# Performance work log

Hardware: AMD Instinct MI355X
Metric: run time of the kernel (lower is better)

## Reference

```python
import jax, jax.numpy as jnp
import numpy as np

H = 32; W = 32; C = 128; K = 3
FS = K * K                      # filter_size = 9
CH = H - K + 1; CW = W - K + 1
F = CH * CW                     # num_convs = 900
HW = H * W                      # 1024
TEMP = 1.0                      # softmax_temp
EPS = 1e-5                      # masked_softmax epsilon
B = 8


def _build_masks():
    # local_indices[f] = flat indices of the K x K window f (row-major),
    # matching compute_input_mask with stride=1, no stochastic stride.
    idx = np.zeros((F, FS), dtype=np.int32)
    f = 0
    for i in range(CH):
        for j in range(CW):
            rows = np.arange(i, i + K)[:, None]
            cols = np.arange(j, j + K)[None, :]
            idx[f] = (rows * W + cols).reshape(-1)
            f += 1
    # global mask = (1 - local_mask) * (1 - padding_mask); padding_mask == 0 for 'valid'
    gmask = np.ones((F, HW), dtype=np.float32)
    gmask[np.arange(F)[:, None], idx] = 0.0
    return jnp.asarray(idx), jnp.asarray(gmask)


def setup_inputs() -> dict:
    key = jax.random.key(0)
    ks = jax.random.split(key, 8)
    bound = 1.0 / np.sqrt(C)  # torch nn.Linear default init
    u = lambda k, shape: jax.random.uniform(k, shape, jnp.float32, -bound, bound)
    batch = jax.random.normal(ks[0], (B, H, W, C), jnp.float32)
    Wq = u(ks[1], (C, C)); bq = u(ks[2], (C,))
    Wk = u(ks[3], (C, C)); bk = u(ks[4], (C,))
    wv = u(ks[5], (C, 1)); bv = u(ks[6], (1,))
    local_indices, gmask = _build_masks()
    return {"batch": batch, "Wq": Wq, "bq": bq, "Wk": Wk, "bk": bk,
            "wv": wv, "bv": bv, "gmask": gmask, "local_indices": local_indices}


def reference(batch, Wq, bq, Wk, bk, wv, bv, gmask, local_indices):
    # Approach '4': per-window local queries attend over global (non-window)
    # pixels; scalar values gate the local patch pixels; gated patch sums to
    # one output pixel per window. Valid padding => local pixels are unmasked
    # and the masked softmax zeroes out window/padding positions, so the
    # per-window masked linear transforms reduce exactly to full-image
    # transforms gathered/masked afterwards (no [F,B,H,W,C] materialization).
    b = batch.shape[0]
    xf = batch.reshape(b, HW, C)
    Q = xf @ Wq.T + bq                         # [B,HW,C] query_transform
    Kf = xf @ Wk.T + bk                        # [B,HW,C] key_transform
    V = (xf @ wv + bv)[..., 0]                 # [B,HW]   value_transform (C->1)
    Qg = Q[:, local_indices]                   # [B,F,FS,C] local queries (gather)
    Xl = xf[:, local_indices]                  # [B,F,FS,C] local patch features
    compat = jnp.einsum('bfpc,bqc->bfpq', Qg, Kf) / TEMP   # [B,F,FS,HW]
    # masked_softmax: exp * mask / (sum + eps), no max-subtraction (faithful)
    exps = jnp.exp(compat) * gmask[None, :, None, :]
    attn = exps / (exps.sum(-1, keepdims=True) + EPS)
    gates = jnp.einsum('bfpq,bq->bfp', attn, V)            # [B,F,FS] scalar gates
    out = jnp.einsum('bfp,bfpc->bfc', gates, Xl)           # [B,F,C]
    return out.reshape(b, CH, CW, C)
```

## Files before the change

### kernel.cpp

```cpp
#include <hip/hip_runtime.h>

#define BATCH 8
#define HW_N  1024
#define CD    128
#define W_IMG 32
#define CH_O  30
#define F_N   900

#define OFF_Q16 0u
#define OFF_K16 2097152u
#define OFF_V   4194304u
#define OFF_D   4227072u
#define OFF_TP  5046272u
#define OFF_TVP 5570560u
#define OFF_WQF 6094848u
#define OFF_WKF 6127616u

typedef _Float16 f16x8 __attribute__((ext_vector_type(8)));
typedef _Float16 f16x4 __attribute__((ext_vector_type(4)));
typedef float    f32x4 __attribute__((ext_vector_type(4)));

__device__ __forceinline__ size_t frag_off(int R, int k) {
    return (size_t)(R >> 4) * 2048 +
           (size_t)((((k >> 5) * 4 + ((k >> 3) & 3)) * 128) + ((R & 15) * 8) + (k & 7));
}

__device__ __forceinline__ void async16(const void* g, void* l) {
    __builtin_amdgcn_global_load_lds(
        (const __attribute__((address_space(1))) unsigned int*)g,
        (__attribute__((address_space(3))) unsigned int*)l,
        16, 0, 0);
}

__global__ __launch_bounds__(256) void prep_kernel(
    const float* __restrict__ Wq, const float* __restrict__ Wk,
    _Float16* __restrict__ WqF, _Float16* __restrict__ WkF)
{
    int id = blockIdx.x * 256 + threadIdx.x;
    int c  = id >> 4;
    int kc = id & 15;
    size_t src = (size_t)c * CD + kc * 8;
    size_t dst = frag_off(c, kc * 8);

    float vq[8], vk[8];
    *(float4*)&vq[0] = *(const float4*)&Wq[src];
    *(float4*)&vq[4] = *(const float4*)&Wq[src + 4];
    *(float4*)&vk[0] = *(const float4*)&Wk[src];
    *(float4*)&vk[4] = *(const float4*)&Wk[src + 4];

    f16x8 qh, kh;
#pragma unroll
    for (int e = 0; e < 8; ++e) {
        qh[e] = (_Float16)vq[e];
        kh[e] = (_Float16)vk[e];
    }
    *(f16x8*)&WqF[dst] = qh;
    *(f16x8*)&WkF[dst] = kh;
}

__global__ __launch_bounds__(256) void qkv_kernel(
    const float* __restrict__ xf,
    const float* __restrict__ bq, const float* __restrict__ bk,
    const float* __restrict__ wv, const float* __restrict__ bv,
    const _Float16* __restrict__ WqF, const _Float16* __restrict__ WkF,
    _Float16* __restrict__ Q16, _Float16* __restrict__ K16,
    float* __restrict__ V)
{
    __shared__ float    xs[16][132];
    __shared__ _Float16 xh[2048];

    const int t = threadIdx.x;
    const int rowbase = blockIdx.x * 16;

#pragma unroll
    for (int m = 0; m < 2; ++m) {
        int id = t + 256 * m;
        int r  = id >> 5;
        int c4 = id & 31;
        float4 v4 = *(const float4*)&xf[(size_t)(rowbase + r) * CD + c4 * 4];
        *(float4*)&xs[r][c4 * 4] = v4;
        int c = c4 * 4;
        int off = ((c >> 5) * 4 + ((c >> 3) & 3)) * 128 + r * 8 + (c & 7);
        f16x4 hh;
        hh[0] = (_Float16)v4.x; hh[1] = (_Float16)v4.y;
        hh[2] = (_Float16)v4.z; hh[3] = (_Float16)v4.w;
        *(f16x4*)&xh[off] = hh;
    }
    __syncthreads();

    const int w    = t >> 6;
    const int lane = t & 63;
    const int q    = lane >> 4;
    const int i    = lane & 15;

    f32x4 aq[2], ak[2];
#pragma unroll
    for (int ct = 0; ct < 2; ++ct) {
        aq[ct] = (f32x4){0.f, 0.f, 0.f, 0.f};
        ak[ct] = (f32x4){0.f, 0.f, 0.f, 0.f};
    }

#pragma unroll
    for (int ks = 0; ks < 4; ++ks) {
        const int aoff = (ks * 4 + q) * 128 + i * 8;
        f16x8 ah = *(f16x8*)&xh[aoff];
#pragma unroll
        for (int ct = 0; ct < 2; ++ct) {
            size_t boff = (size_t)(w * 2 + ct) * 2048 + (size_t)(ks * 4 + q) * 128 + i * 8;
            f16x8 bq8 = *(const f16x8*)&WqF[boff];
            f16x8 bk8 = *(const f16x8*)&WkF[boff];
            aq[ct] = __builtin_amdgcn_mfma_f32_16x16x32_f16(ah, bq8, aq[ct], 0, 0, 0);
            ak[ct] = __builtin_amdgcn_mfma_f32_16x16x32_f16(ah, bk8, ak[ct], 0, 0, 0);
        }
    }

#pragma unroll
    for (int ct = 0; ct < 2; ++ct) {
        int c = (w * 2 + ct) * 16 + i;
        float bqv = bq[c], bkv = bk[c];
#pragma unroll
        for (int g = 0; g < 4; ++g) {
            int R = rowbase + q * 4 + g;
            size_t o = frag_off(R, c);
            Q16[o] = (_Float16)(aq[ct][g] + bqv);
            K16[o] = (_Float16)(ak[ct][g] + bkv);
        }
    }

    if (t < 16) {
        float s = 0.f;
#pragma unroll 8
        for (int k = 0; k < CD; ++k) s += xs[t][k] * wv[k];
        V[rowbase + t] = s + bv[0];
    }
}

#define A_OFF 0
#define B_OFF 16384
#define VS_OFF 32768
#define SCR2 16896
#define ATTN_LDS_TOTAL 33792

__global__ __launch_bounds__(256) void attn_kernel(
    const _Float16* __restrict__ Q16, const _Float16* __restrict__ K16,
    const float* __restrict__ V,
    double* __restrict__ Tp, double* __restrict__ TVp,
    float* __restrict__ D)
{
    extern __shared__ char lds[];
    _Float16* Ah = (_Float16*)(lds + A_OFF);
    _Float16* Bh = (_Float16*)(lds + B_OFF);
    float*    Vs = (float*)(lds + VS_OFF);

    const int b  = blockIdx.x;
    const int rb = blockIdx.y;
    const int cb = blockIdx.z;
    const int t  = threadIdx.x;
    const int w    = t >> 6;
    const int lane = t & 63;
    const int q    = lane >> 4;
    const int i    = lane & 15;
    const int wy = w >> 1, wx = w & 1;

    if (t < 128) Vs[t] = V[b * HW_N + cb * 128 + t];

    f32x4 acc[4][4];
#pragma unroll
    for (int r = 0; r < 4; ++r)
#pragma unroll
        for (int f = 0; f < 4; ++f) acc[r][f] = (f32x4){0.f, 0.f, 0.f, 0.f};

    const size_t abase = (size_t)(b * 8 + rb) * 16384;
    const size_t bbase = (size_t)(b * 8 + cb) * 16384;

    for (int kh = 0; kh < 2; ++kh) {
        __syncthreads();
#pragma unroll
        for (int m = 0; m < 4; ++m) {
            int id = t + 256 * m;
            size_t goff = (size_t)(id >> 7) * 2048 + kh * 1024 + (id & 127) * 8;
            int loff = id * 8;
            async16(Q16 + abase + goff, Ah + loff);
            async16(K16 + bbase + goff, Bh + loff);
        }
        asm volatile("s_waitcnt vmcnt(0)" ::: "memory");
        __syncthreads();

#pragma unroll
        for (int kcl = 0; kcl < 2; ++kcl) {
            f16x8 a4[4], b4[4];
#pragma unroll
            for (int r = 0; r < 4; ++r) {
                int ao = (((wy * 4 + r) * 2 + kcl) * 4 + q) * 128 + i * 8;
                a4[r] = *(f16x8*)&Ah[ao];
                int bo = (((wx * 4 + r) * 2 + kcl) * 4 + q) * 128 + i * 8;
                b4[r] = *(f16x8*)&Bh[bo];
            }
#pragma unroll
            for (int r = 0; r < 4; ++r)
#pragma unroll
                for (int f = 0; f < 4; ++f)
                    acc[r][f] = __builtin_amdgcn_mfma_f32_16x16x32_f16(
                        a4[r], b4[f], acc[r][f], 0, 0, 0);
        }
    }

    float st[4][4], stv[4][4];
#pragma unroll
    for (int r = 0; r < 4; ++r)
#pragma unroll
        for (int g = 0; g < 4; ++g) { st[r][g] = 0.f; stv[r][g] = 0.f; }

    const bool band = (cb - rb <= 1) && (rb - cb <= 1);

#pragma unroll
    for (int f = 0; f < 4; ++f) {
        int col_local = wx * 64 + f * 16 + i;
        int hw_c = cb * 128 + col_local;
        float v = Vs[col_local];
        int cimg_r = hw_c >> 5, cimg_c = hw_c & 31;
#pragma unroll
        for (int r = 0; r < 4; ++r)
#pragma unroll
            for (int g = 0; g < 4; ++g) {
                float e = __expf(acc[r][f][g]);
                st[r][g]  += e;
                stv[r][g] += e * v;
                if (band) {
                    int row_local = wy * 64 + r * 16 + q * 4 + g;
                    int hw_r = rb * 128 + row_local;
                    int dy = cimg_r - (hw_r >> 5);
                    int dx = cimg_c - (hw_r & 31);
                    if ((unsigned)(dy + 2) <= 4u && (unsigned)(dx + 2) <= 4u)
                        D[(size_t)(b * HW_N + hw_r) * 25 + (dy + 2) * 5 + (dx + 2)] = e;
                }
            }
    }

    __syncthreads();
    float* scrT  = (float*)lds;
    float* scrTV = (float*)(lds + SCR2);
#pragma unroll
    for (int r = 0; r < 4; ++r)
#pragma unroll
        for (int g = 0; g < 4; ++g) {
            int rl = wy * 64 + r * 16 + q * 4 + g;
            scrT [rl * 33 + wx * 16 + i] = st[r][g];
            scrTV[rl * 33 + wx * 16 + i] = stv[r][g];
        }
    __syncthreads();
    if (t < 128) {
        double s = 0.0;
#pragma unroll
        for (int c = 0; c < 32; ++c) s += (double)scrT[t * 33 + c];
        Tp[(size_t)(b * HW_N + rb * 128 + t) * 8 + cb] = s;
    } else {
        int tt = t - 128;
        double s = 0.0;
#pragma unroll
        for (int c = 0; c < 32; ++c) s += (double)scrTV[tt * 33 + c];
        TVp[(size_t)(b * HW_N + rb * 128 + tt) * 8 + cb] = s;
    }
}

__global__ __launch_bounds__(256) void gate_out_kernel(
    const float* __restrict__ xf, const float* __restrict__ V,
    const double* __restrict__ Tp, const double* __restrict__ TVp,
    const float* __restrict__ D, float* __restrict__ out)
{
    const int fi = blockIdx.x;
    const int b  = blockIdx.y;
    const int t  = threadIdx.x;

    __shared__ float  xs[96 * 128];
    __shared__ float  gates[32][9];
    __shared__ double Ts[96], TVs[96];

#pragma unroll
    for (int m = 0; m < 12; ++m) {
        int id   = t + 256 * m;
        int srow = id >> 5;
        int c4   = id & 31;
        int r3   = srow >> 5, colc = srow & 31;
        *(float4*)&xs[srow * 128 + c4 * 4] =
            *(const float4*)&xf[((size_t)(b * 32 + fi + r3) * 32 + colc) * CD + c4 * 4];
    }

    if (t < 96) {
        int R = b * HW_N + (fi + (t >> 5)) * W_IMG + (t & 31);
        double s = 0.0;
#pragma unroll
        for (int c = 0; c < 8; ++c) s += Tp[(size_t)R * 8 + c];
        Ts[t] = s;
    } else if (t >= 128 && t < 224) {
        int tt = t - 128;
        int R = b * HW_N + (fi + (tt >> 5)) * W_IMG + (tt & 31);
        double s = 0.0;
#pragma unroll
        for (int c = 0; c < 8; ++c) s += TVp[(size_t)R * 8 + c];
        TVs[tt] = s;
    }
    __syncthreads();

    for (int g = t; g < 270; g += 256) {
        int fj = g / 9, p = g % 9;
        int pr = p / 3, pc = p % 3;
        int lrow = pr * 32 + fj + pc;
        int ip = (fi + pr) * W_IMG + (fj + pc);
        const float* Drow = &D[(size_t)(b * HW_N + ip) * 25];
        double se = 0.0, sev = 0.0;
#pragma unroll
        for (int qq = 0; qq < 9; ++qq) {
            int qr = qq / 3, qc = qq % 3;
            float e = Drow[(qr - pr + 2) * 5 + (qc - pc + 2)];
            se  += (double)e;
            sev += (double)(e * V[b * HW_N + (fi + qr) * W_IMG + (fj + qc)]);
        }
        double denom = Ts[lrow] - se + 1e-5;
        double numer = TVs[lrow] - sev;
        gates[fj][p] = (float)(numer / denom);
    }
    __syncthreads();

    const int c4  = t & 31;
    const int fjl = t >> 5;
#pragma unroll
    for (int it = 0; it < 4; ++it) {
        int fj = fjl + 8 * it;
        if (fj < CH_O) {
            f32x4 o = (f32x4){0.f, 0.f, 0.f, 0.f};
#pragma unroll
            for (int p = 0; p < 9; ++p) {
                int pr = p / 3, pc = p % 3;
                f32x4 x = *(f32x4*)&xs[(pr * 32 + fj + pc) * 128 + c4 * 4];
                float gv = gates[fj][p];
                o += gv * x;
            }
            *(f32x4*)&out[((size_t)(b * F_N) + fi * CH_O + fj) * CD + c4 * 4] = o;
        }
    }
}

extern "C" void kernel_launch(void* const* d_in, const int* in_sizes, int n_in,
                              void* d_out, int out_size, void* d_ws, size_t ws_size,
                              hipStream_t stream)
{
    (void)in_sizes; (void)n_in; (void)out_size; (void)ws_size;
    const float* batch = (const float*)d_in[0];
    const float* Wq    = (const float*)d_in[1];
    const float* bq    = (const float*)d_in[2];
    const float* Wk    = (const float*)d_in[3];
    const float* bk    = (const float*)d_in[4];
    const float* wv    = (const float*)d_in[5];
    const float* bv    = (const float*)d_in[6];

    char*      ws  = (char*)d_ws;
    _Float16*  Q16 = (_Float16*)(ws + OFF_Q16);
    _Float16*  K16 = (_Float16*)(ws + OFF_K16);
    float*     V   = (float*)(ws + OFF_V);
    float*     D   = (float*)(ws + OFF_D);
    double*    Tp  = (double*)(ws + OFF_TP);
    double*    TVp = (double*)(ws + OFF_TVP);
    _Float16*  WqF = (_Float16*)(ws + OFF_WQF);
    _Float16*  WkF = (_Float16*)(ws + OFF_WKF);
    float*     out = (float*)d_out;

    prep_kernel<<<dim3(8), dim3(256), 0, stream>>>(Wq, Wk, WqF, WkF);
    qkv_kernel<<<dim3(512), dim3(256), 0, stream>>>(batch, bq, bk, wv, bv,
                                                    WqF, WkF, Q16, K16, V);
    attn_kernel<<<dim3(8, 8, 8), dim3(256), ATTN_LDS_TOTAL, stream>>>(
        Q16, K16, V, Tp, TVp, D);
    gate_out_kernel<<<dim3(CH_O, BATCH), dim3(256), 0, stream>>>(batch, V, Tp, TVp, D, out);
}
```

Measured before the change: 97.43 us.

## Fuse four kernels into one cooperative persistent kernel with grid syncs

Refactors each of the four stage kernels into device-function bodies and runs them in a single cooperative kernel of 512 blocks, separated by grid.sync(), sharing one dynamic LDS allocation. The aim is to remove the launch gaps and tail idle time between the prep, QKV, attention and gate stages. The original multi-kernel path is kept as a fallback if the cooperative launch fails. In exchange it adds grid-wide barrier cost, forces the largest LDS footprint (about 51 KB) on every stage, and requires all 512 blocks to be co-resident.

```diff
diff --git a/kernel.cpp b/kernel.cpp
--- a/kernel.cpp
+++ b/kernel.cpp
@@ -1,4 +1,7 @@
 #include <hip/hip_runtime.h>
+#include <hip/hip_cooperative_groups.h>
+
+namespace cg = cooperative_groups;
 
 #define BATCH 8
 #define HW_N  1024
@@ -16,6 +19,9 @@
 #define OFF_WQF 6094848u
 #define OFF_WKF 6127616u
 
+#define FUSED_LDS 52224
+#define ATTN_LDS_TOTAL 33792
+
 typedef _Float16 f16x8 __attribute__((ext_vector_type(8)));
 typedef _Float16 f16x4 __attribute__((ext_vector_type(4)));
 typedef float    f32x4 __attribute__((ext_vector_type(4)));
@@ -32,11 +38,12 @@
         16, 0, 0);
 }
 
-__global__ __launch_bounds__(256) void prep_kernel(
+
+__device__ __forceinline__ void prep_body(
+    int id,
     const float* __restrict__ Wq, const float* __restrict__ Wk,
     _Float16* __restrict__ WqF, _Float16* __restrict__ WkF)
 {
-    int id = blockIdx.x * 256 + threadIdx.x;
     int c  = id >> 4;
     int kc = id & 15;
     size_t src = (size_t)c * CD + kc * 8;
@@ -58,7 +65,8 @@
     *(f16x8*)&WkF[dst] = kh;
 }
 
-__global__ __launch_bounds__(256) void qkv_kernel(
+__device__ __forceinline__ void qkv_body(
+    char* smem, int blk, int t,
     const float* __restrict__ xf,
     const float* __restrict__ bq, const float* __restrict__ bk,
     const float* __restrict__ wv, const float* __restrict__ bv,
@@ -66,11 +74,10 @@
     _Float16* __restrict__ Q16, _Float16* __restrict__ K16,
     float* __restrict__ V)
 {
-    __shared__ float    xs[16][132];
-    __shared__ _Float16 xh[2048];
-
-    const int t = threadIdx.x;
-    const int rowbase = blockIdx.x * 16;
+    float*    xs = (float*)smem;
+    _Float16* xh = (_Float16*)(smem + 8448);
+
+    const int rowbase = blk * 16;
 
 #pragma unroll
     for (int m = 0; m < 2; ++m) {
@@ -78,7 +85,7 @@
         int r  = id >> 5;
         int c4 = id & 31;
         float4 v4 = *(const float4*)&xf[(size_t)(rowbase + r) * CD + c4 * 4];
-        *(float4*)&xs[r][c4 * 4] = v4;
+        *(float4*)&xs[r * 132 + c4 * 4] = v4;
         int c = c4 * 4;
         int off = ((c >> 5) * 4 + ((c >> 3) & 3)) * 128 + r * 8 + (c & 7);
         f16x4 hh;
@@ -130,32 +137,22 @@
     if (t < 16) {
         float s = 0.f;
 #pragma unroll 8
-        for (int k = 0; k < CD; ++k) s += xs[t][k] * wv[k];
+        for (int k = 0; k < CD; ++k) s += xs[t * 132 + k] * wv[k];
         V[rowbase + t] = s + bv[0];
     }
 }
 
-#define A_OFF 0
-#define B_OFF 16384
-#define VS_OFF 32768
-#define SCR2 16896
-#define ATTN_LDS_TOTAL 33792
-
-__global__ __launch_bounds__(256) void attn_kernel(
+__device__ __forceinline__ void attn_body(
+    char* smem, int b, int rb, int cb, int t,
     const _Float16* __restrict__ Q16, const _Float16* __restrict__ K16,
     const float* __restrict__ V,
     double* __restrict__ Tp, double* __restrict__ TVp,
     float* __restrict__ D)
 {
-    extern __shared__ char lds[];
-    _Float16* Ah = (_Float16*)(lds + A_OFF);
-    _Float16* Bh = (_Float16*)(lds + B_OFF);
-    float*    Vs = (float*)(lds + VS_OFF);
-
-    const int b  = blockIdx.x;
-    const int rb = blockIdx.y;
-    const int cb = blockIdx.z;
-    const int t  = threadIdx.x;
+    _Float16* Ah = (_Float16*)smem;
+    _Float16* Bh = (_Float16*)(smem + 16384);
+    float*    Vs = (float*)(smem + 32768);
+
     const int w    = t >> 6;
     const int lane = t & 63;
     const int q    = lane >> 4;
@@ -238,8 +235,8 @@
     }
 
     __syncthreads();
-    float* scrT  = (float*)lds;
-    float* scrTV = (float*)(lds + SCR2);
+    float* scrT  = (float*)smem;
+    float* scrTV = (float*)(smem + 16896);
 #pragma unroll
     for (int r = 0; r < 4; ++r)
 #pragma unroll
@@ -263,18 +260,16 @@
     }
 }
 
-__global__ __launch_bounds__(256) void gate_out_kernel(
+__device__ __forceinline__ void gate_body(
+    char* smem, int fi, int b, int t,
     const float* __restrict__ xf, const float* __restrict__ V,
     const double* __restrict__ Tp, const double* __restrict__ TVp,
     const float* __restrict__ D, float* __restrict__ out)
 {
-    const int fi = blockIdx.x;
-    const int b  = blockIdx.y;
-    const int t  = threadIdx.x;
-
-    __shared__ float  xs[96 * 128];
-    __shared__ float  gates[32][9];
-    __shared__ double Ts[96], TVs[96];
+    float*  xs    = (float*)smem;
+    float*  gates = (float*)(smem + 49152);
+    double* Ts    = (double*)(smem + 50304);
+    double* TVs   = (double*)(smem + 51072);
 
 #pragma unroll
     for (int m = 0; m < 12; ++m) {
@@ -318,7 +313,7 @@
         }
         double denom = Ts[lrow] - se + 1e-5;
         double numer = TVs[lrow] - sev;
-        gates[fj][p] = (float)(numer / denom);
+        gates[fj * 9 + p] = (float)(numer / denom);
     }
     __syncthreads();
 
@@ -333,12 +328,83 @@
             for (int p = 0; p < 9; ++p) {
                 int pr = p / 3, pc = p % 3;
                 f32x4 x = *(f32x4*)&xs[(pr * 32 + fj + pc) * 128 + c4 * 4];
-                float gv = gates[fj][p];
+                float gv = gates[fj * 9 + p];
                 o += gv * x;
             }
             *(f32x4*)&out[((size_t)(b * F_N) + fi * CH_O + fj) * CD + c4 * 4] = o;
         }
     }
+}
+
+__global__ __launch_bounds__(256, 2) void fused_kernel(
+    const float* __restrict__ xf,
+    const float* __restrict__ Wq, const float* __restrict__ bq,
+    const float* __restrict__ Wk, const float* __restrict__ bk,
+    const float* __restrict__ wv, const float* __restrict__ bv,
+    _Float16* __restrict__ WqF, _Float16* __restrict__ WkF,
+    _Float16* __restrict__ Q16, _Float16* __restrict__ K16,
+    float* __restrict__ V, float* __restrict__ D,
+    double* __restrict__ Tp, double* __restrict__ TVp,
+    float* __restrict__ out)
+{
+    extern __shared__ char smem[];
+    cg::grid_group grid = cg::this_grid();
+    const int blk = blockIdx.x;
+    const int t   = threadIdx.x;
+
+    if (blk < 8) prep_body(blk * 256 + t, Wq, Wk, WqF, WkF);
+    grid.sync();
+
+    qkv_body(smem, blk, t, xf, bq, bk, wv, bv, WqF, WkF, Q16, K16, V);
+    grid.sync();
+
+    attn_body(smem, blk >> 6, (blk >> 3) & 7, blk & 7, t,
+              Q16, K16, V, Tp, TVp, D);
+    grid.sync();
+
+    if (blk < 240) gate_body(smem, blk % 30, blk / 30, t,
+                             xf, V, Tp, TVp, D, out);
+}
+
+__global__ __launch_bounds__(256) void prep_kernel(
+    const float* __restrict__ Wq, const float* __restrict__ Wk,
+    _Float16* __restrict__ WqF, _Float16* __restrict__ WkF)
+{
+    prep_body(blockIdx.x * 256 + threadIdx.x, Wq, Wk, WqF, WkF);
+}
+
+__global__ __launch_bounds__(256) void qkv_kernel(
+    const float* __restrict__ xf,
+    const float* __restrict__ bq, const float* __restrict__ bk,
+    const float* __restrict__ wv, const float* __restrict__ bv,
+    const _Float16* __restrict__ WqF, const _Float16* __restrict__ WkF,
+    _Float16* __restrict__ Q16, _Float16* __restrict__ K16,
+    float* __restrict__ V)
+{
+    __shared__ char smem[12544];
+    qkv_body(smem, blockIdx.x, threadIdx.x, xf, bq, bk, wv, bv,
+             WqF, WkF, Q16, K16, V);
+}
+
+__global__ __launch_bounds__(256) void attn_kernel(
+    const _Float16* __restrict__ Q16, const _Float16* __restrict__ K16,
+    const float* __restrict__ V,
+    double* __restrict__ Tp, double* __restrict__ TVp,
+    float* __restrict__ D)
+{
+    extern __shared__ char smem[];
+    attn_body(smem, blockIdx.x, blockIdx.y, blockIdx.z, threadIdx.x,
+              Q16, K16, V, Tp, TVp, D);
+}
+
+__global__ __launch_bounds__(256) void gate_out_kernel(
+    const float* __restrict__ xf, const float* __restrict__ V,
+    const double* __restrict__ Tp, const double* __restrict__ TVp,
+    const float* __restrict__ D, float* __restrict__ out)
+{
+    __shared__ char smem[51840];
+    gate_body(smem, blockIdx.x, blockIdx.y, threadIdx.x,
+              xf, V, Tp, TVp, D, out);
 }
 
 extern "C" void kernel_launch(void* const* d_in, const int* in_sizes, int n_in,
@@ -365,10 +431,23 @@
     _Float16*  WkF = (_Float16*)(ws + OFF_WKF);
     float*     out = (float*)d_out;
 
-    prep_kernel<<<dim3(8), dim3(256), 0, stream>>>(Wq, Wk, WqF, WkF);
-    qkv_kernel<<<dim3(512), dim3(256), 0, stream>>>(batch, bq, bk, wv, bv,
-                                                    WqF, WkF, Q16, K16, V);
-    attn_kernel<<<dim3(8, 8, 8), dim3(256), ATTN_LDS_TOTAL, stream>>>(
-        Q16, K16, V, Tp, TVp, D);
-    gate_out_kernel<<<dim3(CH_O, BATCH), dim3(256), 0, stream>>>(batch, V, Tp, TVp, D, out);
-}
+    void* args[] = {
+        (void*)&batch, (void*)&Wq, (void*)&bq, (void*)&Wk, (void*)&bk,
+        (void*)&wv, (void*)&bv, (void*)&WqF, (void*)&WkF,
+        (void*)&Q16, (void*)&K16, (void*)&V, (void*)&D,
+        (void*)&Tp, (void*)&TVp, (void*)&out
+    };
+    hipError_t err = hipLaunchCooperativeKernel(
+        (const void*)fused_kernel, dim3(512), dim3(256),
+        (void**)args, (unsigned)FUSED_LDS, stream);
+
+    if (err != hipSuccess) {
+        prep_kernel<<<dim3(8), dim3(256), 0, stream>>>(Wq, Wk, WqF, WkF);
+        qkv_kernel<<<dim3(512), dim3(256), 0, stream>>>(batch, bq, bk, wv, bv,
+                                                        WqF, WkF, Q16, K16, V);
+        attn_kernel<<<dim3(8, 8, 8), dim3(256), ATTN_LDS_TOTAL, stream>>>(
+            Q16, K16, V, Tp, TVp, D);
+        gate_out_kernel<<<dim3(CH_O, BATCH), dim3(256), 0, stream>>>(
+            batch, V, Tp, TVp, D, out);
+    }
+}
```

Result: slower. 262.7 us (+169.6%).
